# Kernel tuning notes

Hardware: AMD Instinct MI355X
Metric: run time of the kernel (lower is better)

Reference implementation:

```python
import jax, jax.numpy as jnp
import numpy as np
import math

D_MODEL = 1024
EMB = 1024

def setup_inputs() -> dict:
    key = jax.random.key(0)
    ks = jax.random.split(key, 9)
    s = 1.0 / math.sqrt(EMB)
    x = jax.random.normal(ks[0], (4, 2048, EMB), dtype=jnp.float32)
    W1 = jax.random.uniform(ks[1], (EMB, EMB), minval=-s, maxval=s)
    b1 = jax.random.uniform(ks[2], (EMB,), minval=-s, maxval=s)
    W2 = jax.random.uniform(ks[3], (EMB, EMB), minval=-s, maxval=s)
    b2 = jax.random.uniform(ks[4], (EMB,), minval=-s, maxval=s)
    W3 = jax.random.uniform(ks[5], (EMB, EMB), minval=-s, maxval=s)
    b3 = jax.random.uniform(ks[6], (EMB,), minval=-s, maxval=s)
    W4 = jax.random.uniform(ks[7], (EMB, EMB), minval=-s, maxval=s)
    b4 = jax.random.uniform(ks[8], (EMB,), minval=-s, maxval=s)
    return {"x": x, "W1": W1, "b1": b1, "W2": W2, "b2": b2,
            "W3": W3, "b3": b3, "W4": W4, "b4": b4}

def reference(x, W1, b1, W2, b2, W3, b3, W4, b4):
    # Q, K, V projections (torch Linear: x @ W.T + b; here W stored as [in, out])
    Q = x @ W1 + b1          # [B, S, E]
    K = x @ W2 + b2
    V = x @ W3 + b3
    scale = 1.0 / math.sqrt(D_MODEL)
    scores = jnp.einsum('bse,bte->bst', Q, K) * scale   # [B, S, S]
    attn = jax.nn.softmax(scores, axis=-1)
    out = jnp.einsum('bst,bte->bse', attn, V)           # [B, S, E]
    return out @ W4 + b4
```

## Files before the change

### kernel.cpp

```cpp
#include <hip/hip_runtime.h>
#include <hip/hip_bf16.h>

typedef __attribute__((ext_vector_type(4))) float f32x4;
typedef __attribute__((ext_vector_type(8))) short bf16x8;

__device__ __forceinline__ void gload_lds16(const void* g, void* l) {
  __builtin_amdgcn_global_load_lds(
      (const __attribute__((address_space(1))) void*)g,
      (__attribute__((address_space(3))) void*)l, 16, 0, 0);
}

__device__ __forceinline__ unsigned short f2bf(float f) {
  union { float f; unsigned u; } x; x.f = f;
  unsigned r = x.u + 0x7fffu + ((x.u >> 16) & 1u);
  return (unsigned short)(r >> 16);
}

__device__ __forceinline__ float bf2f(unsigned short s) {
  union { unsigned u; float f; } x; x.u = (unsigned)s << 16;
  return x.f;
}

template<int N> __device__ __forceinline__ void vm_wait();
template<> __device__ __forceinline__ void vm_wait<0>() { asm volatile("s_waitcnt vmcnt(0)" ::: "memory"); }
template<> __device__ __forceinline__ void vm_wait<4>() { asm volatile("s_waitcnt vmcnt(4)" ::: "memory"); }
template<> __device__ __forceinline__ void vm_wait<6>() { asm volatile("s_waitcnt vmcnt(6)" ::: "memory"); }

#define BARRIER() asm volatile("s_barrier" ::: "memory")
#define LGKM0()   do { asm volatile("s_waitcnt lgkmcnt(0)" ::: "memory"); \
                       __builtin_amdgcn_sched_barrier(0); } while (0)

template<int BN, int EPI, bool OUT_F32>
__global__ __launch_bounds__(512, 2)
void gemm256(const unsigned short* __restrict__ A,
             const unsigned short* __restrict__ Bt,
             const float* __restrict__ bias,
             float* __restrict__ rs,
             void* __restrict__ Cout,
             int K, int lda, int ldb, int ldc, float alpha,
             long sA, long sB, long sC)
{
  constexpr int THREADS = 512;
  constexpr int WN = BN / 64;
  constexpr int WM = 8 / WN;
  constexpr int WTM = 256 / WM;
  constexpr int M_REP = WTM / 16;
  constexpr int MH = M_REP / 2;
  constexpr int ABUFE = 256 * 64;
  constexpr int BBUFE = BN * 64;
  constexpr int BBASE = 2 * ABUFE;
  constexpr int LOADS_A = 2;
  constexpr int LOADS_B = BN / 128;
  constexpr int VM_STEADY = 2 * LOADS_B + LOADS_A;

  __shared__ __attribute__((aligned(16))) unsigned short lds[BBASE + 2 * BBUFE];

  const int gx = gridDim.x, gy = gridDim.y;
  const int lid = blockIdx.x + gx * (blockIdx.y + gy * blockIdx.z);
  const int nwg = gx * gy * gridDim.z;
  const int q = nwg >> 3, r = nwg & 7;
  const int xcd = lid & 7, idx = lid >> 3;
  const int nl = (xcd < r ? xcd * (q + 1) : r * (q + 1) + (xcd - r) * q) + idx;
  const int bx = nl % gx, by = (nl / gx) % gy, bz = nl / (gx * gy);

  const int tid = threadIdx.x, wave = tid >> 6, lane = tid & 63;
  const int wr = wave / WN, wc = wave % WN;
  const int fr = lane & 15, fq = lane >> 4, sw = fr & 7;

  A  += (size_t)bz * sA;
  Bt += (size_t)bz * sB;
  const int m0 = by * 256;
  const int n0 = bx * BN;
  const int NT = K >> 6;

  f32x4 acc[M_REP][4] = {};
  bf16x8 a[MH][2], b[4][2];

  auto stageA = [&](int t, int half) {
#pragma unroll
    for (int c = 0; c < LOADS_A; ++c) {
      const int s = c * THREADS + tid;
      const int rr = s >> 3;
      const int col = ((tid & 7) ^ (rr & 7)) * 8;
      gload_lds16(A + (size_t)(m0 + half * 128 + rr) * lda + t * 64 + col,
                  &lds[(t & 1) * ABUFE + half * (128 * 64) + s * 8]);
    }
  };
  auto stageB = [&](int t, int half) {
#pragma unroll
    for (int c = 0; c < LOADS_B; ++c) {
      const int s = c * THREADS + tid;
      const int rr = s >> 3;
      const int col = ((tid & 7) ^ (rr & 7)) * 8;
      gload_lds16(Bt + (size_t)(n0 + half * (BN / 2) + rr) * ldb + t * 64 + col,
                  &lds[BBASE + (t & 1) * BBUFE + half * ((BN / 2) * 64) + s * 8]);
    }
  };
  auto readA = [&](int buf, int mq) {
    const unsigned short* p = &lds[buf * ABUFE];
#pragma unroll
    for (int mm = 0; mm < MH; ++mm)
#pragma unroll
      for (int kk = 0; kk < 2; ++kk)
        a[mm][kk] = *(const bf16x8*)(p + (wr * WTM + mq * (WTM / 2) + mm * 16 + fr) * 64
                                       + ((kk * 4 + fq) ^ sw) * 8);
  };
  auto readB = [&](int buf, int nh) {
    const unsigned short* p = &lds[BBASE + buf * BBUFE];
#pragma unroll
    for (int nn = 0; nn < 2; ++nn)
#pragma unroll
      for (int kk = 0; kk < 2; ++kk)
        b[nh * 2 + nn][kk] = *(const bf16x8*)(p + (wc * 64 + (nh * 2 + nn) * 16 + fr) * 64
                                                + ((kk * 4 + fq) ^ sw) * 8);
  };
  auto mfmaQ = [&](int mq, int nh) {
    __builtin_amdgcn_s_setprio(1);
#pragma unroll
    for (int kk = 0; kk < 2; ++kk)
#pragma unroll
      for (int mm = 0; mm < MH; ++mm)
#pragma unroll
        for (int nn = 0; nn < 2; ++nn)
          acc[mq * MH + mm][nh * 2 + nn] = __builtin_amdgcn_mfma_f32_16x16x32_bf16(
              a[mm][kk], b[nh * 2 + nn][kk], acc[mq * MH + mm][nh * 2 + nn], 0, 0, 0);
    __builtin_amdgcn_s_setprio(0);
  };

  stageA(0, 0); stageA(0, 1); stageB(0, 0); stageB(0, 1);
  if (NT > 1) { stageB(1, 0); stageB(1, 1); stageA(1, 0); vm_wait<VM_STEADY>(); }
  else        { vm_wait<0>(); }
  BARRIER();

  for (int t = 0; t < NT; ++t) {
    const int buf = t & 1;
    readA(buf, 0); readB(buf, 0);
    BARRIER(); LGKM0();
    mfmaQ(0, 0);
    BARRIER();
    readB(buf, 1);
    if (t + 1 < NT) stageA(t + 1, 1);
    BARRIER(); LGKM0();
    mfmaQ(0, 1);
    BARRIER();
    readA(buf, 1);
    if (t + 2 < NT) stageB(t + 2, 0);
    BARRIER(); LGKM0();
    mfmaQ(1, 0);
    BARRIER();
    if (t + 2 < NT) { stageB(t + 2, 1); stageA(t + 2, 0); vm_wait<VM_STEADY>(); }
    else            { vm_wait<0>(); }
    BARRIER(); LGKM0();
    mfmaQ(1, 1);
    BARRIER();
  }

  float bvc[4];
  if (EPI == 1) {
#pragma unroll
    for (int nn = 0; nn < 4; ++nn) bvc[nn] = bias[n0 + wc * 64 + nn * 16 + fr];
  }
#pragma unroll
  for (int mm = 0; mm < M_REP; ++mm) {
    const int rbase = m0 + wr * WTM + mm * 16 + fq * 4;
#pragma unroll
    for (int j = 0; j < 4; ++j) {
      const int row = rbase + j;
      float bvr = 0.f, rsc = 1.f;
      if (EPI == 2) bvr = bias[row];
      if (EPI == 4) rsc = __builtin_amdgcn_rcpf(rs[(size_t)bz * 2048 + row]);
      float part = 0.f;
#pragma unroll
      for (int nn = 0; nn < 4; ++nn) {
        const int col = n0 + wc * 64 + nn * 16 + fr;
        float v = acc[mm][nn][j];
        if      (EPI == 1) v = v * alpha + bvc[nn];
        else if (EPI == 2) v = v * alpha + bvr;
        else if (EPI == 3) { v = __expf(v * alpha); part += v; }
        else if (EPI == 4) v = v * rsc;
        else               v = v * alpha;
        const size_t off = (size_t)bz * sC + (size_t)row * ldc + col;
        if (OUT_F32) ((float*)Cout)[off] = v;
        else         ((unsigned short*)Cout)[off] = f2bf(v);
      }
      if (EPI == 3) {
        part += __shfl_xor(part, 1); part += __shfl_xor(part, 2);
        part += __shfl_xor(part, 4); part += __shfl_xor(part, 8);
        if (fr == 0) atomicAdd(rs + (size_t)bz * 2048 + row, part);
      }
    }
  }
}

__global__ __launch_bounds__(256)
void convert_x_kernel(const float* __restrict__ x, unsigned short* __restrict__ xb)
{
  const int idx = (blockIdx.x * 256 + threadIdx.x) * 8;
  const float4 a = *(const float4*)(x + idx);
  const float4 b = *(const float4*)(x + idx + 4);
  unsigned u0 = (unsigned)f2bf(a.x) | ((unsigned)f2bf(a.y) << 16);
  unsigned u1 = (unsigned)f2bf(a.z) | ((unsigned)f2bf(a.w) << 16);
  unsigned u2 = (unsigned)f2bf(b.x) | ((unsigned)f2bf(b.y) << 16);
  unsigned u3 = (unsigned)f2bf(b.z) | ((unsigned)f2bf(b.w) << 16);
  uint4 o; o.x = u0; o.y = u1; o.z = u2; o.w = u3;
  *(uint4*)(xb + idx) = o;
}

__global__ __launch_bounds__(256)
void transpose_w_kernel(const float* __restrict__ Wa, const float* __restrict__ Wb,
                        const float* __restrict__ Wc, const float* __restrict__ Wd,
                        unsigned short* __restrict__ Wt)
{
  __shared__ float t[64][65];
  const float* W = (blockIdx.z == 0) ? Wa : (blockIdx.z == 1) ? Wb
                 : (blockIdx.z == 2) ? Wc : Wd;
  unsigned short* out = Wt + (size_t)blockIdx.z * 1024 * 1024;
  const int k0 = blockIdx.y * 64;
  const int n0 = blockIdx.x * 64;
  const int tx = threadIdx.x & 63, ty = threadIdx.x >> 6;
#pragma unroll
  for (int r = ty; r < 64; r += 4)
    t[r][tx] = W[(size_t)(k0 + r) * 1024 + n0 + tx];
  __syncthreads();
#pragma unroll
  for (int r = ty; r < 64; r += 4)
    out[(size_t)(n0 + r) * 1024 + k0 + tx] = f2bf(t[tx][r]);
}

__global__ __launch_bounds__(256)
void bias_concat_kernel(const float* __restrict__ b1, const float* __restrict__ b2,
                        float* __restrict__ bc)
{
  const int i = blockIdx.x * 256 + threadIdx.x;
  bc[i] = (i < 1024) ? b1[i] : b2[i - 1024];
}

extern "C" void kernel_launch(void* const* d_in, const int* in_sizes, int n_in,
                              void* d_out, int out_size, void* d_ws, size_t ws_size,
                              hipStream_t stream)
{
  const float* x  = (const float*)d_in[0];
  const float* W1 = (const float*)d_in[1];
  const float* b1 = (const float*)d_in[2];
  const float* W2 = (const float*)d_in[3];
  const float* b2 = (const float*)d_in[4];
  const float* W3 = (const float*)d_in[5];
  const float* b3 = (const float*)d_in[6];
  const float* W4 = (const float*)d_in[7];
  const float* b4 = (const float*)d_in[8];

  char* ws = (char*)d_ws;
  const size_t MB = 1024 * 1024;
  unsigned short* xb  = (unsigned short*)(ws);
  unsigned short* Wt  = (unsigned short*)(ws + 16 * MB);
  unsigned short* QK  = (unsigned short*)(ws + 24 * MB);
  unsigned short* Vt  = (unsigned short*)(ws + 56 * MB);
  unsigned short* S   = (unsigned short*)(ws + 72 * MB);
  float*          bc  = (float*)S;
  float*          rsum = (float*)ws;
  unsigned short* O   = QK;

  convert_x_kernel<<<4096, 256, 0, stream>>>(x, xb);
  transpose_w_kernel<<<dim3(16, 16, 4), 256, 0, stream>>>(W1, W2, W3, W4, Wt);
  bias_concat_kernel<<<8, 256, 0, stream>>>(b1, b2, bc);

  gemm256<256, 1, false><<<dim3(8, 32, 1), 512, 0, stream>>>(
      xb, Wt, bc, nullptr, QK, 1024, 1024, 1024, 2048, 1.f, 0, 0, 0);

  gemm256<128, 2, false><<<dim3(16, 4, 4), 512, 0, stream>>>(
      Wt + 2 * 1048576, xb, b3, nullptr, Vt, 1024, 1024, 1024, 2048, 1.f,
      0, 2048L * 1024, 1024L * 2048);

  hipMemsetAsync(rsum, 0, 4 * 2048 * sizeof(float), stream);

  gemm256<256, 3, false><<<dim3(8, 8, 4), 512, 0, stream>>>(
      QK, QK + 1024, nullptr, rsum, S, 1024, 2048, 2048, 2048, 0.03125f,
      2048L * 2048, 2048L * 2048, 2048L * 2048);

  gemm256<128, 4, false><<<dim3(8, 8, 4), 512, 0, stream>>>(
      S, Vt, nullptr, rsum, O, 2048, 2048, 2048, 1024, 1.f,
      2048L * 2048, 1024L * 2048, 2048L * 1024);

  gemm256<128, 1, true><<<dim3(8, 32, 1), 512, 0, stream>>>(
      O, Wt + 3 * 1048576, b4, nullptr, d_out, 1024, 1024, 1024, 1024, 1.f,
      0, 0, 0);
}
```

Measured before the change: 194.6 us.

## Fold W3·W4 and the biases to eliminate the output projection GEMM

```diff
diff --git a/kernel.cpp b/kernel.cpp
--- a/kernel.cpp
+++ b/kernel.cpp
@@ -27,8 +27,7 @@
 template<> __device__ __forceinline__ void vm_wait<6>() { asm volatile("s_waitcnt vmcnt(6)" ::: "memory"); }
 
 #define BARRIER() asm volatile("s_barrier" ::: "memory")
-#define LGKM0()   do { asm volatile("s_waitcnt lgkmcnt(0)" ::: "memory"); \
-                       __builtin_amdgcn_sched_barrier(0); } while (0)
+#define SCHED0()  __builtin_amdgcn_sched_barrier(0)
 
 template<int BN, int EPI, bool OUT_F32>
 __global__ __launch_bounds__(512, 2)
@@ -135,28 +134,32 @@
   for (int t = 0; t < NT; ++t) {
     const int buf = t & 1;
     readA(buf, 0); readB(buf, 0);
-    BARRIER(); LGKM0();
+    BARRIER(); SCHED0();
     mfmaQ(0, 0);
+    SCHED0();
     BARRIER();
     readB(buf, 1);
     if (t + 1 < NT) stageA(t + 1, 1);
-    BARRIER(); LGKM0();
+    BARRIER(); SCHED0();
     mfmaQ(0, 1);
+    SCHED0();
     BARRIER();
     readA(buf, 1);
     if (t + 2 < NT) stageB(t + 2, 0);
-    BARRIER(); LGKM0();
+    BARRIER(); SCHED0();
     mfmaQ(1, 0);
+    SCHED0();
     BARRIER();
     if (t + 2 < NT) { stageB(t + 2, 1); stageA(t + 2, 0); vm_wait<VM_STEADY>(); }
     else            { vm_wait<0>(); }
-    BARRIER(); LGKM0();
+    BARRIER(); SCHED0();
     mfmaQ(1, 1);
+    SCHED0();
     BARRIER();
   }
 
   float bvc[4];
-  if (EPI == 1) {
+  if (EPI == 1 || EPI == 5) {
 #pragma unroll
     for (int nn = 0; nn < 4; ++nn) bvc[nn] = bias[n0 + wc * 64 + nn * 16 + fr];
   }
@@ -168,7 +171,7 @@
       const int row = rbase + j;
       float bvr = 0.f, rsc = 1.f;
       if (EPI == 2) bvr = bias[row];
-      if (EPI == 4) rsc = __builtin_amdgcn_rcpf(rs[(size_t)bz * 2048 + row]);
+      if (EPI == 5) rsc = __builtin_amdgcn_rcpf(rs[(size_t)bz * 2048 + row]);
       float part = 0.f;
 #pragma unroll
       for (int nn = 0; nn < 4; ++nn) {
@@ -177,11 +180,12 @@
         if      (EPI == 1) v = v * alpha + bvc[nn];
         else if (EPI == 2) v = v * alpha + bvr;
         else if (EPI == 3) { v = __expf(v * alpha); part += v; }
-        else if (EPI == 4) v = v * rsc;
+        else if (EPI == 5) v = v * rsc + bvc[nn];
         else               v = v * alpha;
         const size_t off = (size_t)bz * sC + (size_t)row * ldc + col;
-        if (OUT_F32) ((float*)Cout)[off] = v;
-        else         ((unsigned short*)Cout)[off] = f2bf(v);
+        if      (EPI == 6) atomicAdd((float*)Cout + off, v);
+        else if (OUT_F32)  ((float*)Cout)[off] = v;
+        else               ((unsigned short*)Cout)[off] = f2bf(v);
       }
       if (EPI == 3) {
         part += __shfl_xor(part, 1); part += __shfl_xor(part, 2);
@@ -193,7 +197,7 @@
 }
 
 __global__ __launch_bounds__(256)
-void convert_x_kernel(const float* __restrict__ x, unsigned short* __restrict__ xb)
+void convert_kernel(const float* __restrict__ x, unsigned short* __restrict__ xb)
 {
   const int idx = (blockIdx.x * 256 + threadIdx.x) * 8;
   const float4 a = *(const float4*)(x + idx);
@@ -208,12 +212,11 @@
 
 __global__ __launch_bounds__(256)
 void transpose_w_kernel(const float* __restrict__ Wa, const float* __restrict__ Wb,
-                        const float* __restrict__ Wc, const float* __restrict__ Wd,
+                        const float* __restrict__ Wc,
                         unsigned short* __restrict__ Wt)
 {
   __shared__ float t[64][65];
-  const float* W = (blockIdx.z == 0) ? Wa : (blockIdx.z == 1) ? Wb
-                 : (blockIdx.z == 2) ? Wc : Wd;
+  const float* W = (blockIdx.z == 0) ? Wa : (blockIdx.z == 1) ? Wb : Wc;
   unsigned short* out = Wt + (size_t)blockIdx.z * 1024 * 1024;
   const int k0 = blockIdx.y * 64;
   const int n0 = blockIdx.x * 64;
@@ -233,6 +236,25 @@
 {
   const int i = blockIdx.x * 256 + threadIdx.x;
   bc[i] = (i < 1024) ? b1[i] : b2[i - 1024];
+}
+
+__global__ __launch_bounds__(256)
+void bias_fold_kernel(const unsigned short* __restrict__ W4t,
+                      const float* __restrict__ b3,
+                      const float* __restrict__ b4,
+                      float* __restrict__ bf)
+{
+  const int e = blockIdx.x * 4 + (threadIdx.x >> 6);
+  const int lane = threadIdx.x & 63;
+  float acc = 0.f;
+#pragma unroll 4
+  for (int i = 0; i < 16; ++i) {
+    const int j = i * 64 + lane;
+    acc += bf2f(W4t[(size_t)e * 1024 + j]) * b3[j];
+  }
+#pragma unroll
+  for (int o = 32; o; o >>= 1) acc += __shfl_xor(acc, o);
+  if (lane == 0) bf[e] = acc + b4[e];
 }
 
 extern "C" void kernel_launch(void* const* d_in, const int* in_sizes, int n_in,
@@ -251,37 +273,46 @@
 
   char* ws = (char*)d_ws;
   const size_t MB = 1024 * 1024;
-  unsigned short* xb  = (unsigned short*)(ws);
-  unsigned short* Wt  = (unsigned short*)(ws + 16 * MB);
-  unsigned short* QK  = (unsigned short*)(ws + 24 * MB);
-  unsigned short* Vt  = (unsigned short*)(ws + 56 * MB);
-  unsigned short* S   = (unsigned short*)(ws + 72 * MB);
-  float*          bc  = (float*)S;
+  unsigned short* xb   = (unsigned short*)(ws);
+  unsigned short* Wt   = (unsigned short*)(ws + 16 * MB);
+  unsigned short* QK   = (unsigned short*)(ws + 24 * MB);
+  unsigned short* Vt   = (unsigned short*)(ws + 56 * MB);
+  unsigned short* S    = (unsigned short*)(ws + 72 * MB);
+  unsigned short* W3b  = (unsigned short*)(ws + 72 * MB);
+  float*          W34f = (float*)(ws + 74 * MB);
+  unsigned short* W34t = (unsigned short*)(ws + 78 * MB);
+  float*          bc   = (float*)(ws + 80 * MB);
   float*          rsum = (float*)ws;
-  unsigned short* O   = QK;
-
-  convert_x_kernel<<<4096, 256, 0, stream>>>(x, xb);
-  transpose_w_kernel<<<dim3(16, 16, 4), 256, 0, stream>>>(W1, W2, W3, W4, Wt);
+  float*          bfv  = (float*)(ws + 32 * 1024);
+
+  unsigned short* W4t = Wt + 2 * 1048576;
+
+  convert_kernel<<<4096, 256, 0, stream>>>(x, xb);
+  transpose_w_kernel<<<dim3(16, 16, 3), 256, 0, stream>>>(W1, W2, W4, Wt);
+  convert_kernel<<<512, 256, 0, stream>>>(W3, W3b);
   bias_concat_kernel<<<8, 256, 0, stream>>>(b1, b2, bc);
+
+  hipMemsetAsync(W34f, 0, 1024 * 1024 * sizeof(float), stream);
+  gemm256<128, 6, true><<<dim3(8, 4, 4), 512, 0, stream>>>(
+      W4t, W3b, nullptr, nullptr, W34f, 256, 1024, 1024, 1024, 1.f,
+      256, 256, 0);
+  convert_kernel<<<512, 256, 0, stream>>>(W34f, W34t);
 
   gemm256<256, 1, false><<<dim3(8, 32, 1), 512, 0, stream>>>(
       xb, Wt, bc, nullptr, QK, 1024, 1024, 1024, 2048, 1.f, 0, 0, 0);
 
-  gemm256<128, 2, false><<<dim3(16, 4, 4), 512, 0, stream>>>(
-      Wt + 2 * 1048576, xb, b3, nullptr, Vt, 1024, 1024, 1024, 2048, 1.f,
+  gemm256<128, 0, false><<<dim3(16, 4, 4), 512, 0, stream>>>(
+      W34t, xb, nullptr, nullptr, Vt, 1024, 1024, 1024, 2048, 1.f,
       0, 2048L * 1024, 1024L * 2048);
 
   hipMemsetAsync(rsum, 0, 4 * 2048 * sizeof(float), stream);
+  bias_fold_kernel<<<256, 256, 0, stream>>>(W4t, b3, b4, bfv);
 
   gemm256<256, 3, false><<<dim3(8, 8, 4), 512, 0, stream>>>(
       QK, QK + 1024, nullptr, rsum, S, 1024, 2048, 2048, 2048, 0.03125f,
       2048L * 2048, 2048L * 2048, 2048L * 2048);
 
-  gemm256<128, 4, false><<<dim3(8, 8, 4), 512, 0, stream>>>(
-      S, Vt, nullptr, rsum, O, 2048, 2048, 2048, 1024, 1.f,
+  gemm256<128, 5, true><<<dim3(8, 8, 4), 512, 0, stream>>>(
+      S, Vt, bfv, rsum, d_out, 2048, 2048, 2048, 1024, 1.f,
       2048L * 2048, 1024L * 2048, 2048L * 1024);
-
-  gemm256<128, 1, true><<<dim3(8, 32, 1), 512, 0, stream>>>(
-      O, Wt + 3 * 1048576, b4, nullptr, d_out, 1024, 1024, 1024, 1024, 1.f,
-      0, 0, 0);
-}
+}
```

Result: slower. 198.8 us (+2.2%).
